# Performance work log

Measured on AMD Instinct MI355X. Metric: run time of the kernel, lower is better.

The kernel has to match this reference:

```python
import jax, jax.numpy as jnp
import numpy as np

N_NODES = 100000
N_EDGES = 2000000
N_GRAPHS = 1000
DIM = 32
NUM_FEATURES = 7
NUM_CLASSES = 2
BN_EPS = 1e-5


def setup_inputs() -> dict:
    key = jax.random.key(0)
    ks = jax.random.split(key, 24)
    inp = {
        "x": jax.random.normal(ks[0], (N_NODES, NUM_FEATURES), dtype=jnp.float32),
        "edge_index": jax.random.randint(ks[1], (2, N_EDGES), 0, N_NODES, dtype=jnp.int64),
        "batch": jnp.sort(jax.random.randint(ks[2], (N_NODES,), 0, N_GRAPHS, dtype=jnp.int64)),
        "conv1_W1": jax.random.normal(ks[3], (NUM_FEATURES, DIM), dtype=jnp.float32) * 0.3,
        "conv1_b1": jax.random.normal(ks[4], (DIM,), dtype=jnp.float32) * 0.1,
        "conv1_W2": jax.random.normal(ks[5], (DIM, DIM), dtype=jnp.float32) * 0.15,
        "conv1_b2": jax.random.normal(ks[6], (DIM,), dtype=jnp.float32) * 0.1,
        "convs_W1": jax.random.normal(ks[7], (4, DIM, DIM), dtype=jnp.float32) * 0.15,
        "convs_b1": jax.random.normal(ks[8], (4, DIM), dtype=jnp.float32) * 0.1,
        "convs_W2": jax.random.normal(ks[9], (4, DIM, DIM), dtype=jnp.float32) * 0.15,
        "convs_b2": jax.random.normal(ks[10], (4, DIM), dtype=jnp.float32) * 0.1,
        "bn_gamma": jax.random.uniform(ks[11], (5, DIM), dtype=jnp.float32, minval=0.5, maxval=1.5),
        "bn_beta": jax.random.normal(ks[12], (5, DIM), dtype=jnp.float32) * 0.1,
        "bn_mean": jax.random.normal(ks[13], (5, DIM), dtype=jnp.float32) * 0.1,
        "bn_var": jax.random.uniform(ks[14], (5, DIM), dtype=jnp.float32, minval=0.5, maxval=1.5),
        "fc1_W": jax.random.normal(ks[15], (DIM, DIM), dtype=jnp.float32) * 0.15,
        "fc1_b": jax.random.normal(ks[16], (DIM,), dtype=jnp.float32) * 0.1,
        "fc2_W": jax.random.normal(ks[17], (DIM, NUM_CLASSES), dtype=jnp.float32) * 0.15,
        "fc2_b": jax.random.normal(ks[18], (NUM_CLASSES,), dtype=jnp.float32) * 0.1,
    }
    return inp


def _gin_conv(h, src, dst, W1, b1, W2, b2):
    # GINConv with eps=0: nn((1+eps)*x + sum_{j in N(i)} x_j)
    agg = jax.ops.segment_sum(h[src], dst, num_segments=N_NODES)
    z = h + agg
    z = jnp.maximum(z @ W1 + b1, 0.0)
    return z @ W2 + b2


def _bn_eval(h, gamma, beta, mean, var):
    return (h - mean) * jax.lax.rsqrt(var + BN_EPS) * gamma + beta


def reference(x, edge_index, batch,
              conv1_W1, conv1_b1, conv1_W2, conv1_b2,
              convs_W1, convs_b1, convs_W2, convs_b2,
              bn_gamma, bn_beta, bn_mean, bn_var,
              fc1_W, fc1_b, fc2_W, fc2_b):
    src, dst = edge_index[0], edge_index[1]
    h = _gin_conv(x, src, dst, conv1_W1, conv1_b1, conv1_W2, conv1_b2)
    h = jnp.maximum(h, 0.0)
    h = _bn_eval(h, bn_gamma[0], bn_beta[0], bn_mean[0], bn_var[0])
    for i in range(4):  # conv2..conv5
        h = _gin_conv(h, src, dst, convs_W1[i], convs_b1[i], convs_W2[i], convs_b2[i])
        h = jnp.maximum(h, 0.0)
        h = _bn_eval(h, bn_gamma[i + 1], bn_beta[i + 1], bn_mean[i + 1], bn_var[i + 1])
    # global add pool over graphs
    g = jax.ops.segment_sum(h, batch, num_segments=N_GRAPHS)  # [G, DIM]
    g = jnp.maximum(g @ fc1_W + fc1_b, 0.0)
    # dropout: eval mode -> identity
    logits = g @ fc2_W + fc2_b
    return jax.nn.log_softmax(logits, axis=-1)
```

## Files before the change

kernel.cpp:

```cpp
#include <hip/hip_runtime.h>

#define N_NODES  100000
#define N_EDGES  2000000
#define N_GRAPHS 1000
#define NFEAT    7
#define BN_EPS   1e-5f
#define MAXDEG   64

#define BSH      7
#define NBKT     782
#define BCAP     3584
#define E_PER_BLK 4096
#define NGRP     6250

__device__ __forceinline__ unsigned bf16_rne(float f) {
  unsigned u = __float_as_uint(f);
  return (u + 0x7FFFu + ((u >> 16) & 1u)) >> 16;
}
__device__ __forceinline__ float bf_lo(unsigned u) { return __uint_as_float(u << 16); }
__device__ __forceinline__ float bf_hi(unsigned u) { return __uint_as_float(u & 0xFFFF0000u); }

__global__ __launch_bounds__(1024) void b1_bucket(const int* __restrict__ src,
                                                  const int* __restrict__ dst,
                                                  int* __restrict__ gCur,
                                                  unsigned* __restrict__ ebuf) {
  __shared__ int hist[NBKT], base[NBKT];
  int tid = threadIdx.x;
  for (int i = tid; i < NBKT; i += 1024) hist[i] = 0;
  __syncthreads();
  unsigned pk[4];
  int bo[4];
  int e0 = blockIdx.x * E_PER_BLK;
#pragma unroll
  for (int k = 0; k < 4; ++k) {
    int e = e0 + k * 1024 + tid;
    if (e < N_EDGES) {
      int d = dst[e], s = src[e];
      int b = d >> BSH;
      int off = atomicAdd(&hist[b], 1);
      pk[k] = ((unsigned)(d & 127) << 17) | (unsigned)s;
      bo[k] = (b << 17) | off;
    } else {
      bo[k] = -1;
    }
  }
  __syncthreads();
  for (int i = tid; i < NBKT; i += 1024)
    base[i] = hist[i] ? atomicAdd(&gCur[i], hist[i]) : 0;
  __syncthreads();
#pragma unroll
  for (int k = 0; k < 4; ++k) {
    if (bo[k] >= 0) {
      int b = bo[k] >> 17, off = bo[k] & 0x1FFFF;
      int p = base[b] + off;
      if (p < BCAP) ebuf[(size_t)b * BCAP + p] = pk[k];
    }
  }
}

__global__ __launch_bounds__(512) void b2_csr(const unsigned* __restrict__ ebuf,
                                              const int* __restrict__ gCnt,
                                              int* __restrict__ cnt,
                                              int* __restrict__ csr,
                                              int* __restrict__ gmax) {
  __shared__ int hist[128];
  __shared__ int stage[128 * MAXDEG];
  int b = blockIdx.x, tid = threadIdx.x;
  if (tid < 128) hist[tid] = 0;
  for (int i = tid; i < 128 * MAXDEG; i += 512) stage[i] = (b << BSH) + (i >> 6);
  __syncthreads();
  int n = gCnt[b];
  if (n > BCAP) n = BCAP;
  const unsigned* eb = ebuf + (size_t)b * BCAP;
  for (int i = tid; i < n; i += 512) {
    unsigned pk = eb[i];
    int dloc = (int)(pk >> 17);
    int slot = atomicAdd(&hist[dloc], 1);
    if (slot < MAXDEG) stage[(dloc << 6) + slot] = (int)(pk & 0x1FFFFu);
  }
  __syncthreads();
  if (tid < 128) {
    int gnode = (b << BSH) + tid;
    if (gnode < N_NODES) cnt[gnode] = hist[tid];
  }
  if (tid < 8) {
    int mx = 1;
#pragma unroll
    for (int k = 0; k < 16; ++k) {
      int d = hist[tid * 16 + k];
      if (d > 63) d = 63;
      if (d + 1 > mx) mx = d + 1;
    }
    gmax[(b << 3) + tid] = mx;
  }
  const int4* st4 = (const int4*)stage;
  int4* dst4 = (int4*)(csr + (size_t)b * (128 * MAXDEG));
  for (int i = tid; i < 128 * MAXDEG / 4; i += 512) dst4[i] = st4[i];
}

__global__ __launch_bounds__(256) void xcvt_kernel(const float* __restrict__ x,
                                                   unsigned* __restrict__ xc) {
  int i = blockIdx.x * 256 + threadIdx.x;
  if (i >= N_NODES * 4) return;
  int n = i >> 2, p = i & 3;
  float lo = x[n * 7 + 2 * p];
  float hi = (2 * p + 1 < 7) ? x[n * 7 + 2 * p + 1] : 0.f;
  xc[i] = bf16_rne(lo) | (bf16_rne(hi) << 16);
}

__global__ __launch_bounds__(256) void gin1(
    const unsigned short* __restrict__ xc16, const int* __restrict__ cnt,
    const int* __restrict__ csr,
    const float* __restrict__ W1, const float* __restrict__ b1,
    const float* __restrict__ W2, const float* __restrict__ b2,
    const float* __restrict__ gamma, const float* __restrict__ beta,
    const float* __restrict__ mean, const float* __restrict__ var,
    unsigned short* __restrict__ hout16) {
  __shared__ __align__(16) float zsA[4][8], zsB[4][8];
  __shared__ __align__(16) float tsA[4][32], tsB[4][32];
  int tid = threadIdx.x;
  int w = __builtin_amdgcn_readfirstlane(tid >> 6);
  int lane = tid & 63;
  int grp = lane >> 2;
  int ch  = lane & 3;
  int half = lane >> 5, j = lane & 31;

  float wr1[4], wr2[16];
#pragma unroll
  for (int i = 0; i < 4; ++i) {
    int k = half * 4 + i;
    wr1[i] = (k < 7) ? W1[k * 32 + j] : 0.f;
  }
#pragma unroll
  for (int i = 0; i < 16; ++i) wr2[i] = W2[(half * 16 + i) * 32 + j];
  float vb1 = b1[j], vb2 = b2[j];
  float sc = gamma[j] * rsqrtf(var[j] + BN_EPS);
  float sh = beta[j] - mean[j] * sc;

  const unsigned* xc32 = (const unsigned*)xc16;

  const int NW = gridDim.x * 4;
  const int NPAIR = N_NODES / 2;
  for (int pr = blockIdx.x * 4 + w; pr < NPAIR; pr += NW) {
    int n0 = 2 * pr, n1 = n0 + 1;
    int d0 = cnt[n0];
    int d1 = cnt[n1];
    if (d0 > 63) d0 = 63;
    if (d1 > 63) d1 = 63;
    int dE0 = d0 + 1, dE1 = d1 + 1;

    int idx0 = (lane < d0) ? csr[n0 * MAXDEG + lane] : n0;
    int idx1 = (lane < d1) ? csr[n1 * MAXDEG + lane] : n1;

    unsigned vA[4], vB[4];
#pragma unroll
    for (int s = 0; s < 4; ++s) {
      int sidA = __shfl(idx0, s * 16 + grp);
      vA[s] = xc32[(size_t)sidA * 4 + ch];
    }
#pragma unroll
    for (int s = 0; s < 4; ++s) {
      int sidB = __shfl(idx1, s * 16 + grp);
      vB[s] = xc32[(size_t)sidB * 4 + ch];
    }

    float a0 = 0.f, a1 = 0.f;
    float c0 = 0.f, c1 = 0.f;
#pragma unroll
    for (int s = 0; s < 4; ++s) {
      int e = s * 16 + grp;
      if (e < dE0) { a0 += bf_lo(vA[s]); a1 += bf_hi(vA[s]); }
      if (e < dE1) { c0 += bf_lo(vB[s]); c1 += bf_hi(vB[s]); }
    }
#pragma unroll
    for (int m = 4; m <= 32; m <<= 1) {
      a0 += __shfl_xor(a0, m); a1 += __shfl_xor(a1, m);
      c0 += __shfl_xor(c0, m); c1 += __shfl_xor(c1, m);
    }
    if (grp == 0) {
      float2 za = {a0, a1};
      float2 zc = {c0, c1};
      *(float2*)&zsA[w][ch * 2] = za;
      *(float2*)&zsB[w][ch * 2] = zc;
    }

    float tp = half ? 0.f : vb1;
    {
      const float4* zp = (const float4*)&zsA[w][half * 4];
      float4 z0 = zp[0];
      tp = fmaf(z0.x, wr1[0], tp); tp = fmaf(z0.y, wr1[1], tp);
      tp = fmaf(z0.z, wr1[2], tp); tp = fmaf(z0.w, wr1[3], tp);
    }
    tp += __shfl_xor(tp, 32);
    tp = fmaxf(tp, 0.f);
    if (!half) tsA[w][j] = tp;

    float op = half ? 0.f : vb2;
    {
      const float4* tpp = (const float4*)&tsA[w][half * 16];
      float4 t0 = tpp[0], t1 = tpp[1], t2 = tpp[2], t3 = tpp[3];
      op = fmaf(t0.x, wr2[0], op);  op = fmaf(t0.y, wr2[1], op);
      op = fmaf(t0.z, wr2[2], op);  op = fmaf(t0.w, wr2[3], op);
      op = fmaf(t1.x, wr2[4], op);  op = fmaf(t1.y, wr2[5], op);
      op = fmaf(t1.z, wr2[6], op);  op = fmaf(t1.w, wr2[7], op);
      op = fmaf(t2.x, wr2[8], op);  op = fmaf(t2.y, wr2[9], op);
      op = fmaf(t2.z, wr2[10], op); op = fmaf(t2.w, wr2[11], op);
      op = fmaf(t3.x, wr2[12], op); op = fmaf(t3.y, wr2[13], op);
      op = fmaf(t3.z, wr2[14], op); op = fmaf(t3.w, wr2[15], op);
    }
    op += __shfl_xor(op, 32);
    if (!half) {
      op = fmaxf(op, 0.f) * sc + sh;
      float hi = __shfl(op, j | 1);
      if ((j & 1) == 0) {
        unsigned pk = bf16_rne(op) | (bf16_rne(hi) << 16);
        ((unsigned*)hout16)[n0 * 16 + (j >> 1)] = pk;
      }
    }

    float tq = half ? 0.f : vb1;
    {
      const float4* zp = (const float4*)&zsB[w][half * 4];
      float4 z0 = zp[0];
      tq = fmaf(z0.x, wr1[0], tq); tq = fmaf(z0.y, wr1[1], tq);
      tq = fmaf(z0.z, wr1[2], tq); tq = fmaf(z0.w, wr1[3], tq);
    }
    tq += __shfl_xor(tq, 32);
    tq = fmaxf(tq, 0.f);
    if (!half) tsB[w][j] = tq;

    float oq = half ? 0.f : vb2;
    {
      const float4* tpp = (const float4*)&tsB[w][half * 16];
      float4 t0 = tpp[0], t1 = tpp[1], t2 = tpp[2], t3 = tpp[3];
      oq = fmaf(t0.x, wr2[0], oq);  oq = fmaf(t0.y, wr2[1], oq);
      oq = fmaf(t0.z, wr2[2], oq);  oq = fmaf(t0.w, wr2[3], oq);
      oq = fmaf(t1.x, wr2[4], oq);  oq = fmaf(t1.y, wr2[5], oq);
      oq = fmaf(t1.z, wr2[6], oq);  oq = fmaf(t1.w, wr2[7], oq);
      oq = fmaf(t2.x, wr2[8], oq);  oq = fmaf(t2.y, wr2[9], oq);
      oq = fmaf(t2.z, wr2[10], oq); oq = fmaf(t2.w, wr2[11], oq);
      oq = fmaf(t3.x, wr2[12], oq); oq = fmaf(t3.y, wr2[13], oq);
      oq = fmaf(t3.z, wr2[14], oq); oq = fmaf(t3.w, wr2[15], oq);
    }
    oq += __shfl_xor(oq, 32);
    if (!half) {
      oq = fmaxf(oq, 0.f) * sc + sh;
      float hi = __shfl(oq, j | 1);
      if ((j & 1) == 0) {
        unsigned pk = bf16_rne(oq) | (bf16_rne(hi) << 16);
        ((unsigned*)hout16)[n1 * 16 + (j >> 1)] = pk;
      }
    }
  }
}

__global__ __launch_bounds__(256) void gin_layer32(
    const unsigned short* __restrict__ hin16, const int* __restrict__ cnt,
    const int* __restrict__ csr, const int* __restrict__ gmax,
    const float* __restrict__ W1, const float* __restrict__ b1,
    const float* __restrict__ W2, const float* __restrict__ b2,
    const float* __restrict__ gamma, const float* __restrict__ beta,
    const float* __restrict__ mean, const float* __restrict__ var,
    unsigned short* __restrict__ hout16) {
  __shared__ __align__(16) float zs[4][16][36];
  __shared__ __align__(16) float ts[4][32];
  int tid = threadIdx.x;
  int w = __builtin_amdgcn_readfirstlane(tid >> 6);
  int lane = tid & 63;
  int nl = lane & 15;
  int c  = lane >> 4;
  int half = lane >> 5, j = lane & 31;

  float wr1[16], wr2[16];
#pragma unroll
  for (int i = 0; i < 16; ++i) wr1[i] = W1[(half * 16 + i) * 32 + j];
#pragma unroll
  for (int i = 0; i < 16; ++i) wr2[i] = W2[(half * 16 + i) * 32 + j];
  float vb1 = b1[j], vb2 = b2[j];
  float sc = gamma[j] * rsqrtf(var[j] + BN_EPS);
  float sh = beta[j] - mean[j] * sc;

  const int NW = gridDim.x * 4;
  for (int g = blockIdx.x * 4 + w; g < NGRP; g += NW) {
    int node = g * 16 + nl;
    int dcnt = cnt[node];
    if (dcnt > 63) dcnt = 63;
    int dE = dcnt + 1;
    int dmax = __builtin_amdgcn_readfirstlane(gmax[g]);
    int nb = (dmax + 3) >> 2;

    const int* crow = csr + (size_t)node * MAXDEG;
    float acc[8];
#pragma unroll
    for (int i = 0; i < 8; ++i) acc[i] = 0.f;

    uint4 i4 = *(const uint4*)crow;
    for (int b = 0; b < nb; ++b) {
      uint4 i4n = i4;
      if (b + 1 < nb) i4n = *(const uint4*)(crow + (b + 1) * 4);
      uint4 v0 = *(const uint4*)(hin16 + (size_t)i4.x * 32 + c * 8);
      uint4 v1 = *(const uint4*)(hin16 + (size_t)i4.y * 32 + c * 8);
      uint4 v2 = *(const uint4*)(hin16 + (size_t)i4.z * 32 + c * 8);
      uint4 v3 = *(const uint4*)(hin16 + (size_t)i4.w * 32 + c * 8);
      int s0 = b * 4;
      if (s0 + 0 < dE) {
        acc[0] += bf_lo(v0.x); acc[1] += bf_hi(v0.x);
        acc[2] += bf_lo(v0.y); acc[3] += bf_hi(v0.y);
        acc[4] += bf_lo(v0.z); acc[5] += bf_hi(v0.z);
        acc[6] += bf_lo(v0.w); acc[7] += bf_hi(v0.w);
      }
      if (s0 + 1 < dE) {
        acc[0] += bf_lo(v1.x); acc[1] += bf_hi(v1.x);
        acc[2] += bf_lo(v1.y); acc[3] += bf_hi(v1.y);
        acc[4] += bf_lo(v1.z); acc[5] += bf_hi(v1.z);
        acc[6] += bf_lo(v1.w); acc[7] += bf_hi(v1.w);
      }
      if (s0 + 2 < dE) {
        acc[0] += bf_lo(v2.x); acc[1] += bf_hi(v2.x);
        acc[2] += bf_lo(v2.y); acc[3] += bf_hi(v2.y);
        acc[4] += bf_lo(v2.z); acc[5] += bf_hi(v2.z);
        acc[6] += bf_lo(v2.w); acc[7] += bf_hi(v2.w);
      }
      if (s0 + 3 < dE) {
        acc[0] += bf_lo(v3.x); acc[1] += bf_hi(v3.x);
        acc[2] += bf_lo(v3.y); acc[3] += bf_hi(v3.y);
        acc[4] += bf_lo(v3.z); acc[5] += bf_hi(v3.z);
        acc[6] += bf_lo(v3.w); acc[7] += bf_hi(v3.w);
      }
      i4 = i4n;
    }

    {
      float4 z0 = {acc[0], acc[1], acc[2], acc[3]};
      float4 z1 = {acc[4], acc[5], acc[6], acc[7]};
      *(float4*)&zs[w][nl][c * 8]     = z0;
      *(float4*)&zs[w][nl][c * 8 + 4] = z1;
    }

    for (int p = 0; p < 16; ++p) {
      int np = g * 16 + p;
      float tp = half ? 0.f : vb1;
      {
        const float4* zp = (const float4*)&zs[w][p][half * 16];
        float4 q0 = zp[0], q1 = zp[1], q2 = zp[2], q3 = zp[3];
        tp = fmaf(q0.x, wr1[0], tp);  tp = fmaf(q0.y, wr1[1], tp);
        tp = fmaf(q0.z, wr1[2], tp);  tp = fmaf(q0.w, wr1[3], tp);
        tp = fmaf(q1.x, wr1[4], tp);  tp = fmaf(q1.y, wr1[5], tp);
        tp = fmaf(q1.z, wr1[6], tp);  tp = fmaf(q1.w, wr1[7], tp);
        tp = fmaf(q2.x, wr1[8], tp);  tp = fmaf(q2.y, wr1[9], tp);
        tp = fmaf(q2.z, wr1[10], tp); tp = fmaf(q2.w, wr1[11], tp);
        tp = fmaf(q3.x, wr1[12], tp); tp = fmaf(q3.y, wr1[13], tp);
        tp = fmaf(q3.z, wr1[14], tp); tp = fmaf(q3.w, wr1[15], tp);
      }
      tp += __shfl_xor(tp, 32);
      tp = fmaxf(tp, 0.f);
      if (!half) ts[w][j] = tp;

      float op = half ? 0.f : vb2;
      {
        const float4* tpp = (const float4*)&ts[w][half * 16];
        float4 q0 = tpp[0], q1 = tpp[1], q2 = tpp[2], q3 = tpp[3];
        op = fmaf(q0.x, wr2[0], op);  op = fmaf(q0.y, wr2[1], op);
        op = fmaf(q0.z, wr2[2], op);  op = fmaf(q0.w, wr2[3], op);
        op = fmaf(q1.x, wr2[4], op);  op = fmaf(q1.y, wr2[5], op);
        op = fmaf(q1.z, wr2[6], op);  op = fmaf(q1.w, wr2[7], op);
        op = fmaf(q2.x, wr2[8], op);  op = fmaf(q2.y, wr2[9], op);
        op = fmaf(q2.z, wr2[10], op); op = fmaf(q2.w, wr2[11], op);
        op = fmaf(q3.x, wr2[12], op); op = fmaf(q3.y, wr2[13], op);
        op = fmaf(q3.z, wr2[14], op); op = fmaf(q3.w, wr2[15], op);
      }
      op += __shfl_xor(op, 32);
      if (!half) {
        op = fmaxf(op, 0.f) * sc + sh;
        float hi = __shfl(op, j | 1);
        if ((j & 1) == 0) {
          unsigned pk = bf16_rne(op) | (bf16_rne(hi) << 16);
          ((unsigned*)hout16)[np * 16 + (j >> 1)] = pk;
        }
      }
    }
  }
}

__global__ __launch_bounds__(256) void pool_kernel(const unsigned short* __restrict__ h16,
                                                   const int* __restrict__ batch,
                                                   float* __restrict__ g) {
  __shared__ int s_lo, s_hi;
  __shared__ float red[8][33];
  int gr = blockIdx.x;
  if (threadIdx.x == 0) {
    int lo = 0, hi = N_NODES;
    while (lo < hi) { int m = (lo + hi) >> 1; if (batch[m] < gr) lo = m + 1; else hi = m; }
    s_lo = lo;
  } else if (threadIdx.x == 1) {
    int lo = 0, hi = N_NODES;
    while (lo < hi) { int m = (lo + hi) >> 1; if (batch[m] < gr + 1) lo = m + 1; else hi = m; }
    s_hi = lo;
  }
  __syncthreads();
  int lo = s_lo, hi = s_hi;
  int j = threadIdx.x & 31;
  int nd = threadIdx.x >> 5;
  float acc = 0.f;
  for (int n = lo + nd; n < hi; n += 8)
    acc += __uint_as_float((unsigned)h16[n * 32 + j] << 16);
  red[nd][j] = acc;
  __syncthreads();
  if (threadIdx.x < 32) {
    float s = 0.f;
#pragma unroll
    for (int r = 0; r < 8; ++r) s += red[r][j];
    g[gr * 32 + j] = s;
  }
}

__global__ __launch_bounds__(256) void head_kernel(
    const float* __restrict__ g, const float* __restrict__ W1, const float* __restrict__ b1,
    const float* __restrict__ W2, const float* __restrict__ b2, float* __restrict__ out) {
  __shared__ float sW1[1024], sb1[32];
  __shared__ float sW2[64], sb2[2];
  __shared__ float zb[8][33], tb[8][33], lb[8][2];
  int tid = threadIdx.x;
  for (int i = tid; i < 1024; i += 256) sW1[i] = W1[i];
  if (tid < 64) sW2[tid] = W2[tid];
  if (tid < 32) sb1[tid] = b1[tid];
  if (tid < 2) sb2[tid] = b2[tid];
  int nd = tid >> 5;
  int gr = blockIdx.x * 8 + nd;
  int j = tid & 31;
  __syncthreads();
  float z = (gr < N_GRAPHS) ? g[gr * 32 + j] : 0.f;
  zb[nd][j] = z;
  __syncthreads();
  float t = sb1[j];
#pragma unroll
  for (int k = 0; k < 32; ++k) t = fmaf(zb[nd][k], sW1[k * 32 + j], t);
  t = fmaxf(t, 0.f);
  tb[nd][j] = t;
  __syncthreads();
  if (j < 2) {
    float l = sb2[j];
#pragma unroll
    for (int k = 0; k < 32; ++k) l = fmaf(tb[nd][k], sW2[k * 2 + j], l);
    lb[nd][j] = l;
  }
  __syncthreads();
  if (gr < N_GRAPHS && j < 2) {
    float l0 = lb[nd][0], l1 = lb[nd][1];
    float m = fmaxf(l0, l1);
    float lse = m + logf(expf(l0 - m) + expf(l1 - m));
    out[gr * 2 + j] = lb[nd][j] - lse;
  }
}

extern "C" void kernel_launch(void* const* d_in, const int* in_sizes, int n_in,
                              void* d_out, int out_size, void* d_ws, size_t ws_size,
                              hipStream_t stream) {
  const float* x     = (const float*)d_in[0];
  const int*   eidx  = (const int*)d_in[1];
  const int*   batch = (const int*)d_in[2];
  const float* c1W1  = (const float*)d_in[3];
  const float* c1b1  = (const float*)d_in[4];
  const float* c1W2  = (const float*)d_in[5];
  const float* c1b2  = (const float*)d_in[6];
  const float* csW1  = (const float*)d_in[7];
  const float* csb1  = (const float*)d_in[8];
  const float* csW2  = (const float*)d_in[9];
  const float* csb2  = (const float*)d_in[10];
  const float* bng   = (const float*)d_in[11];
  const float* bnb   = (const float*)d_in[12];
  const float* bnm   = (const float*)d_in[13];
  const float* bnv   = (const float*)d_in[14];
  const float* fc1W  = (const float*)d_in[15];
  const float* fc1b  = (const float*)d_in[16];
  const float* fc2W  = (const float*)d_in[17];
  const float* fc2b  = (const float*)d_in[18];
  float* out = (float*)d_out;

  const int* src = eidx;
  const int* dst = eidx + N_EDGES;

  char* p = (char*)d_ws;
  unsigned short* hA16 = (unsigned short*)p; p += (size_t)N_NODES * 32 * 2;
  unsigned short* hB16 = (unsigned short*)p; p += (size_t)N_NODES * 32 * 2;
  int*      cnt  = (int*)p;      p += (size_t)N_NODES * 4;
  int*      csr  = (int*)p;      p += (size_t)NBKT * 128 * MAXDEG * 4;
  unsigned* ebuf = (unsigned*)p; p += (size_t)NBKT * BCAP * 4;
  int*      gCur = (int*)p;      p += 1024 * 4;
  int*      gmax = (int*)p;      p += (size_t)(NBKT * 8) * 4;
  float*    g    = (float*)p;    p += (size_t)N_GRAPHS * 32 * 4;
  unsigned* xc = ebuf;

  (void)hipMemsetAsync(gCur, 0, 1024 * 4, stream);
  b1_bucket<<<(N_EDGES + E_PER_BLK - 1) / E_PER_BLK, 1024, 0, stream>>>(src, dst, gCur, ebuf);
  b2_csr<<<NBKT, 512, 0, stream>>>(ebuf, gCur, cnt, csr, gmax);

  xcvt_kernel<<<(N_NODES * 4 + 255) / 256, 256, 0, stream>>>(x, xc);

  gin1<<<2048, 256, 0, stream>>>(
      (const unsigned short*)xc, cnt, csr, c1W1, c1b1, c1W2, c1b2,
      bng, bnb, bnm, bnv, hA16);

  unsigned short* cur = hA16;
  unsigned short* nxt = hB16;
  for (int i = 0; i < 4; ++i) {
    gin_layer32<<<(NGRP + 3) / 4, 256, 0, stream>>>(
        cur, cnt, csr, gmax,
        csW1 + (size_t)i * 1024, csb1 + (size_t)i * 32,
        csW2 + (size_t)i * 1024, csb2 + (size_t)i * 32,
        bng + (size_t)(i + 1) * 32, bnb + (size_t)(i + 1) * 32,
        bnm + (size_t)(i + 1) * 32, bnv + (size_t)(i + 1) * 32, nxt);
    unsigned short* tmp = cur; cur = nxt; nxt = tmp;
  }

  pool_kernel<<<N_GRAPHS, 256, 0, stream>>>(cur, batch, g);
  head_kernel<<<(N_GRAPHS + 7) / 8, 256, 0, stream>>>(g, fc1W, fc1b, fc2W, fc2b, out);
}
```

Before: 342.9 us.

## Restructure first GIN layer to process 16-node groups with per-lane CSR gathers

The first GIN layer now gives each wavefront a group of 16 nodes instead of a pair. Each of the 16 nodes gets 4 lanes, one per feature channel, and those lanes walk the node's CSR row with vectorized 4-index loads, bounded by the group max degree from gmax. The aggregated features are staged in shared memory, and the MLP runs node by node over the group. This removes the per-pair shuffles and the wasted fixed-width 64-slot gather, in exchange for a serialized per-node MLP loop and sensitivity to degree imbalance within a group.

```diff
diff --git a/kernel.cpp b/kernel.cpp
--- a/kernel.cpp
+++ b/kernel.cpp
@@ -110,19 +110,19 @@
 
 __global__ __launch_bounds__(256) void gin1(
     const unsigned short* __restrict__ xc16, const int* __restrict__ cnt,
-    const int* __restrict__ csr,
+    const int* __restrict__ csr, const int* __restrict__ gmax,
     const float* __restrict__ W1, const float* __restrict__ b1,
     const float* __restrict__ W2, const float* __restrict__ b2,
     const float* __restrict__ gamma, const float* __restrict__ beta,
     const float* __restrict__ mean, const float* __restrict__ var,
     unsigned short* __restrict__ hout16) {
-  __shared__ __align__(16) float zsA[4][8], zsB[4][8];
-  __shared__ __align__(16) float tsA[4][32], tsB[4][32];
+  __shared__ __align__(16) float zs[4][16][12];
+  __shared__ __align__(16) float ts[4][32];
   int tid = threadIdx.x;
   int w = __builtin_amdgcn_readfirstlane(tid >> 6);
   int lane = tid & 63;
-  int grp = lane >> 2;
-  int ch  = lane & 3;
+  int nl = lane & 15;
+  int c  = lane >> 4;
   int half = lane >> 5, j = lane & 31;
 
   float wr1[4], wr2[16];
@@ -140,115 +140,72 @@
   const unsigned* xc32 = (const unsigned*)xc16;
 
   const int NW = gridDim.x * 4;
-  const int NPAIR = N_NODES / 2;
-  for (int pr = blockIdx.x * 4 + w; pr < NPAIR; pr += NW) {
-    int n0 = 2 * pr, n1 = n0 + 1;
-    int d0 = cnt[n0];
-    int d1 = cnt[n1];
-    if (d0 > 63) d0 = 63;
-    if (d1 > 63) d1 = 63;
-    int dE0 = d0 + 1, dE1 = d1 + 1;
-
-    int idx0 = (lane < d0) ? csr[n0 * MAXDEG + lane] : n0;
-    int idx1 = (lane < d1) ? csr[n1 * MAXDEG + lane] : n1;
-
-    unsigned vA[4], vB[4];
-#pragma unroll
-    for (int s = 0; s < 4; ++s) {
-      int sidA = __shfl(idx0, s * 16 + grp);
-      vA[s] = xc32[(size_t)sidA * 4 + ch];
-    }
-#pragma unroll
-    for (int s = 0; s < 4; ++s) {
-      int sidB = __shfl(idx1, s * 16 + grp);
-      vB[s] = xc32[(size_t)sidB * 4 + ch];
-    }
-
+  for (int g = blockIdx.x * 4 + w; g < NGRP; g += NW) {
+    int node = g * 16 + nl;
+    int dcnt = cnt[node];
+    if (dcnt > 63) dcnt = 63;
+    int dE = dcnt + 1;
+    int dmax = __builtin_amdgcn_readfirstlane(gmax[g]);
+    int nb = (dmax + 3) >> 2;
+
+    const int* crow = csr + (size_t)node * MAXDEG;
     float a0 = 0.f, a1 = 0.f;
-    float c0 = 0.f, c1 = 0.f;
-#pragma unroll
-    for (int s = 0; s < 4; ++s) {
-      int e = s * 16 + grp;
-      if (e < dE0) { a0 += bf_lo(vA[s]); a1 += bf_hi(vA[s]); }
-      if (e < dE1) { c0 += bf_lo(vB[s]); c1 += bf_hi(vB[s]); }
-    }
-#pragma unroll
-    for (int m = 4; m <= 32; m <<= 1) {
-      a0 += __shfl_xor(a0, m); a1 += __shfl_xor(a1, m);
-      c0 += __shfl_xor(c0, m); c1 += __shfl_xor(c1, m);
-    }
-    if (grp == 0) {
-      float2 za = {a0, a1};
-      float2 zc = {c0, c1};
-      *(float2*)&zsA[w][ch * 2] = za;
-      *(float2*)&zsB[w][ch * 2] = zc;
-    }
-
-    float tp = half ? 0.f : vb1;
+
+    uint4 i4 = *(const uint4*)crow;
+    for (int b = 0; b < nb; ++b) {
+      uint4 i4n = i4;
+      if (b + 1 < nb) i4n = *(const uint4*)(crow + (b + 1) * 4);
+      unsigned v0 = xc32[(size_t)i4.x * 4 + c];
+      unsigned v1 = xc32[(size_t)i4.y * 4 + c];
+      unsigned v2 = xc32[(size_t)i4.z * 4 + c];
+      unsigned v3 = xc32[(size_t)i4.w * 4 + c];
+      int s0 = b * 4;
+      if (s0 + 0 < dE) { a0 += bf_lo(v0); a1 += bf_hi(v0); }
+      if (s0 + 1 < dE) { a0 += bf_lo(v1); a1 += bf_hi(v1); }
+      if (s0 + 2 < dE) { a0 += bf_lo(v2); a1 += bf_hi(v2); }
+      if (s0 + 3 < dE) { a0 += bf_lo(v3); a1 += bf_hi(v3); }
+      i4 = i4n;
+    }
+
     {
-      const float4* zp = (const float4*)&zsA[w][half * 4];
-      float4 z0 = zp[0];
-      tp = fmaf(z0.x, wr1[0], tp); tp = fmaf(z0.y, wr1[1], tp);
-      tp = fmaf(z0.z, wr1[2], tp); tp = fmaf(z0.w, wr1[3], tp);
-    }
-    tp += __shfl_xor(tp, 32);
-    tp = fmaxf(tp, 0.f);
-    if (!half) tsA[w][j] = tp;
-
-    float op = half ? 0.f : vb2;
-    {
-      const float4* tpp = (const float4*)&tsA[w][half * 16];
-      float4 t0 = tpp[0], t1 = tpp[1], t2 = tpp[2], t3 = tpp[3];
-      op = fmaf(t0.x, wr2[0], op);  op = fmaf(t0.y, wr2[1], op);
-      op = fmaf(t0.z, wr2[2], op);  op = fmaf(t0.w, wr2[3], op);
-      op = fmaf(t1.x, wr2[4], op);  op = fmaf(t1.y, wr2[5], op);
-      op = fmaf(t1.z, wr2[6], op);  op = fmaf(t1.w, wr2[7], op);
-      op = fmaf(t2.x, wr2[8], op);  op = fmaf(t2.y, wr2[9], op);
-      op = fmaf(t2.z, wr2[10], op); op = fmaf(t2.w, wr2[11], op);
-      op = fmaf(t3.x, wr2[12], op); op = fmaf(t3.y, wr2[13], op);
-      op = fmaf(t3.z, wr2[14], op); op = fmaf(t3.w, wr2[15], op);
-    }
-    op += __shfl_xor(op, 32);
-    if (!half) {
-      op = fmaxf(op, 0.f) * sc + sh;
-      float hi = __shfl(op, j | 1);
-      if ((j & 1) == 0) {
-        unsigned pk = bf16_rne(op) | (bf16_rne(hi) << 16);
-        ((unsigned*)hout16)[n0 * 16 + (j >> 1)] = pk;
-      }
-    }
-
-    float tq = half ? 0.f : vb1;
-    {
-      const float4* zp = (const float4*)&zsB[w][half * 4];
-      float4 z0 = zp[0];
-      tq = fmaf(z0.x, wr1[0], tq); tq = fmaf(z0.y, wr1[1], tq);
-      tq = fmaf(z0.z, wr1[2], tq); tq = fmaf(z0.w, wr1[3], tq);
-    }
-    tq += __shfl_xor(tq, 32);
-    tq = fmaxf(tq, 0.f);
-    if (!half) tsB[w][j] = tq;
-
-    float oq = half ? 0.f : vb2;
-    {
-      const float4* tpp = (const float4*)&tsB[w][half * 16];
-      float4 t0 = tpp[0], t1 = tpp[1], t2 = tpp[2], t3 = tpp[3];
-      oq = fmaf(t0.x, wr2[0], oq);  oq = fmaf(t0.y, wr2[1], oq);
-      oq = fmaf(t0.z, wr2[2], oq);  oq = fmaf(t0.w, wr2[3], oq);
-      oq = fmaf(t1.x, wr2[4], oq);  oq = fmaf(t1.y, wr2[5], oq);
-      oq = fmaf(t1.z, wr2[6], oq);  oq = fmaf(t1.w, wr2[7], oq);
-      oq = fmaf(t2.x, wr2[8], oq);  oq = fmaf(t2.y, wr2[9], oq);
-      oq = fmaf(t2.z, wr2[10], oq); oq = fmaf(t2.w, wr2[11], oq);
-      oq = fmaf(t3.x, wr2[12], oq); oq = fmaf(t3.y, wr2[13], oq);
-      oq = fmaf(t3.z, wr2[14], oq); oq = fmaf(t3.w, wr2[15], oq);
-    }
-    oq += __shfl_xor(oq, 32);
-    if (!half) {
-      oq = fmaxf(oq, 0.f) * sc + sh;
-      float hi = __shfl(oq, j | 1);
-      if ((j & 1) == 0) {
-        unsigned pk = bf16_rne(oq) | (bf16_rne(hi) << 16);
-        ((unsigned*)hout16)[n1 * 16 + (j >> 1)] = pk;
+      float2 z0 = {a0, a1};
+      *(float2*)&zs[w][nl][c * 2] = z0;
+    }
+
+    for (int p = 0; p < 16; ++p) {
+      int np = g * 16 + p;
+      float tp = half ? 0.f : vb1;
+      {
+        const float4* zp = (const float4*)&zs[w][p][half * 4];
+        float4 z0 = zp[0];
+        tp = fmaf(z0.x, wr1[0], tp); tp = fmaf(z0.y, wr1[1], tp);
+        tp = fmaf(z0.z, wr1[2], tp); tp = fmaf(z0.w, wr1[3], tp);
+      }
+      tp += __shfl_xor(tp, 32);
+      tp = fmaxf(tp, 0.f);
+      if (!half) ts[w][j] = tp;
+
+      float op = half ? 0.f : vb2;
+      {
+        const float4* tpp = (const float4*)&ts[w][half * 16];
+        float4 t0 = tpp[0], t1 = tpp[1], t2 = tpp[2], t3 = tpp[3];
+        op = fmaf(t0.x, wr2[0], op);  op = fmaf(t0.y, wr2[1], op);
+        op = fmaf(t0.z, wr2[2], op);  op = fmaf(t0.w, wr2[3], op);
+        op = fmaf(t1.x, wr2[4], op);  op = fmaf(t1.y, wr2[5], op);
+        op = fmaf(t1.z, wr2[6], op);  op = fmaf(t1.w, wr2[7], op);
+        op = fmaf(t2.x, wr2[8], op);  op = fmaf(t2.y, wr2[9], op);
+        op = fmaf(t2.z, wr2[10], op); op = fmaf(t2.w, wr2[11], op);
+        op = fmaf(t3.x, wr2[12], op); op = fmaf(t3.y, wr2[13], op);
+        op = fmaf(t3.z, wr2[14], op); op = fmaf(t3.w, wr2[15], op);
+      }
+      op += __shfl_xor(op, 32);
+      if (!half) {
+        op = fmaxf(op, 0.f) * sc + sh;
+        float hi = __shfl(op, j | 1);
+        if ((j & 1) == 0) {
+          unsigned pk = bf16_rne(op) | (bf16_rne(hi) << 16);
+          ((unsigned*)hout16)[np * 16 + (j >> 1)] = pk;
+        }
       }
     }
   }
@@ -497,8 +454,8 @@
 
   xcvt_kernel<<<(N_NODES * 4 + 255) / 256, 256, 0, stream>>>(x, xc);
 
-  gin1<<<2048, 256, 0, stream>>>(
-      (const unsigned short*)xc, cnt, csr, c1W1, c1b1, c1W2, c1b2,
+  gin1<<<(NGRP + 3) / 4, 256, 0, stream>>>(
+      (const unsigned short*)xc, cnt, csr, gmax, c1W1, c1b1, c1W2, c1b2,
       bng, bnb, bnm, bnv, hA16);
 
   unsigned short* cur = hA16;
```

Result: no change. 341.9 us (-0.3%).
